# Optimization experiments

Measured on AMD Instinct MI355X. Metric: run time of the kernel, lower is better.

Reference implementation:

```python
import jax, jax.numpy as jnp
import numpy as np

N_NODES = 50000
N_EDGES = 800000
IN_CH, HID_CH, OUT_CH = 512, 256, 128


def setup_inputs() -> dict:
    key = jax.random.key(0)
    k = jax.random.split(key, 6)
    x = jax.random.normal(k[0], (N_NODES, IN_CH), dtype=jnp.float32)
    edge_index = jax.random.randint(k[1], (2, N_EDGES), 0, N_NODES, dtype=jnp.int64)
    # Glorot-ish scaled weights
    W0 = jax.random.normal(k[2], (IN_CH, HID_CH), dtype=jnp.float32) * (1.0 / np.sqrt(IN_CH))
    b0 = jnp.zeros((HID_CH,), dtype=jnp.float32)
    W1 = jax.random.normal(k[3], (HID_CH, OUT_CH), dtype=jnp.float32) * (1.0 / np.sqrt(HID_CH))
    b1 = jnp.zeros((OUT_CH,), dtype=jnp.float32)
    PW = jax.random.normal(k[4], (OUT_CH, OUT_CH), dtype=jnp.float32) * (1.0 / np.sqrt(OUT_CH))
    Pb = jnp.zeros((OUT_CH,), dtype=jnp.float32)
    return {"x": x, "edge_index": edge_index, "W0": W0, "b0": b0,
            "W1": W1, "b1": b1, "PW": PW, "Pb": Pb}


def reference(x, edge_index, W0, b0, W1, b1, PW, Pb):
    N = x.shape[0]
    # GCN normalization with added self-loops (edge_weight=None -> ones)
    loop = jnp.arange(N, dtype=edge_index.dtype)
    src = jnp.concatenate([edge_index[0], loop])  # [E+N]
    dst = jnp.concatenate([edge_index[1], loop])
    w = jnp.ones(src.shape[0], dtype=x.dtype)
    deg = jax.ops.segment_sum(w, dst, num_segments=N)  # in-degree incl. self-loop
    dinv = jnp.where(deg > 0, jax.lax.rsqrt(jnp.maximum(deg, 1e-12)), 0.0)
    norm = dinv[src] * dinv[dst]  # [E+N]

    def gcn_conv(h, W, b):
        hl = h @ W                               # [N, F_out] linear first (PyG GCNConv)
        msg = norm[:, None] * hl[src]            # gather + scale  [E+N, F_out]
        return jax.ops.segment_sum(msg, dst, num_segments=N) + b

    # eval mode: dropout is identity
    h = jax.nn.relu(gcn_conv(x, W0, b0))
    h = gcn_conv(h, W1, b1)                      # last layer: no relu
    p = h @ PW + Pb                              # PGE linear [N, OUT]
    vals = jnp.max(p, axis=0)                    # torch.max(dim=0) -> (values, indices)
    idx = jnp.argmax(p, axis=0)
    return (h, vals, idx)
```

## Files before the change

kernel.cpp:

```cpp
#include <hip/hip_runtime.h>
#include <stdint.h>

#define N_NODES 50000
#define N_EDGES 800000
#define IN_CH   512
#define HID_CH  256
#define OUT_CH  128
#define NPAD    50048
#define SLOT    96

#define NB_E   3125
#define NB2    391

#define PBKT  NB_E
#define PW0B  (PBKT + 64)
#define PW1B  (PW0B + 16)
#define PPWB  (PW1B + 8)

typedef unsigned short ushort_t;
typedef __attribute__((ext_vector_type(8))) short    short8;
typedef __attribute__((ext_vector_type(4))) float    floatx4;
typedef __attribute__((ext_vector_type(4))) _Float16 half4v;
typedef __attribute__((ext_vector_type(2))) _Float16 half2v;

__device__ inline ushort_t f2bf(float x) {
    union { float f; unsigned u; } v; v.f = x;
    unsigned r = v.u + 0x7fffu + ((v.u >> 16) & 1u);
    return (ushort_t)(r >> 16);
}
__device__ inline float bf2f(ushort_t h) {
    union { unsigned u; float f; } v; v.u = ((unsigned)h) << 16;
    return v.f;
}
__device__ inline void gl_lds16(const void* g, void* l) {
    __builtin_amdgcn_global_load_lds((const __attribute__((address_space(1))) void*)g,
                                     (__attribute__((address_space(3))) void*)l, 16, 0, 0);
}

#define SWZ(r) ((((r) >> 1) & 3) << 3)

#define SYNC_PIPE(N) do {                                                    \
    asm volatile("s_waitcnt vmcnt(" #N ") lgkmcnt(0)" ::: "memory");         \
    __builtin_amdgcn_sched_barrier(0);                                       \
    __builtin_amdgcn_s_barrier();                                            \
    __builtin_amdgcn_sched_barrier(0); } while (0)

__device__ inline void conv_splitT8(const float* __restrict__ W,
                                    ushort_t* __restrict__ WhT,
                                    ushort_t* __restrict__ WlT,
                                    int K, int N, int base) {
    float4 v0 = *(const float4*)(W + base);
    float4 v1 = *(const float4*)(W + base + 4);
    float vv[8] = {v0.x, v0.y, v0.z, v0.w, v1.x, v1.y, v1.z, v1.w};
    #pragma unroll
    for (int j = 0; j < 8; ++j) {
        int g = base + j;
        int k = g / N, n = g - k * N;
        int ks = k ^ SWZ(n);
        ushort_t h = f2bf(vv[j]);
        WhT[(size_t)n * K + ks] = h;
        WlT[(size_t)n * K + ks] = f2bf(vv[j] - bf2f(h));
    }
}

__global__ __launch_bounds__(256) void k_prep(const int* __restrict__ esrc,
                                              const int* __restrict__ edst,
                                              const float* __restrict__ W0,
                                              const float* __restrict__ W1,
                                              const float* __restrict__ PW,
                                              int* __restrict__ cnt,
                                              int* __restrict__ slots,
                                              ushort_t* W0hT, ushort_t* W0lT,
                                              ushort_t* W1hT, ushort_t* W1lT,
                                              ushort_t* PWhT, ushort_t* PWlT) {
    int b = blockIdx.x, tid = threadIdx.x;
    if (b < PBKT) {
        int e = b * 256 + tid;
        if (e < N_EDGES) {
            int d = edst[e];
            int c = atomicAdd(&cnt[d], 1);
            slots[(size_t)d * SLOT + c] = esrc[e];
        }
    } else if (b < PW0B) {
        conv_splitT8(W0, W0hT, W0lT, IN_CH, HID_CH, (b - PBKT) * 2048 + tid * 8);
    } else if (b < PW1B) {
        conv_splitT8(W1, W1hT, W1lT, HID_CH, OUT_CH, (b - PW0B) * 2048 + tid * 8);
    } else {
        conv_splitT8(PW, PWhT, PWlT, OUT_CH, OUT_CH, (b - PW1B) * 2048 + tid * 8);
    }
}

__global__ __launch_bounds__(256) void k_dinv(const int* __restrict__ cnt,
                                              float* __restrict__ dinv) {
    int i = blockIdx.x * 256 + threadIdx.x;
    if (i < N_NODES) dinv[i] = rsqrtf((float)cnt[i] + 1.0f);
}

__global__ __launch_bounds__(256, 2) void gemm0_x(const float* __restrict__ A,
                                                  const ushort_t* __restrict__ BhT,
                                                  const ushort_t* __restrict__ BlT,
                                                  const float* __restrict__ dinv,
                                                  _Float16* __restrict__ C,
                                                  int M, int N) {
    constexpr int KT = IN_CH;
    constexpr int NT = KT / 32;
    __shared__ ushort_t sm[2][4][128 * 32];
    const int tid  = threadIdx.x;
    const int wave = tid >> 6, lane = tid & 63;
    const int m0 = blockIdx.y * 128, n0 = blockIdx.x * 128;

    const int sr = tid >> 1, sseg = tid & 1;
    const float* gA = A + (size_t)min(m0 + sr, M - 1) * KT + sseg * 16;
    const int swa = (sr >> 1) & 3;
    const int wo0 = sr * 32 + (((sseg * 2)     ^ swa) * 8);
    const int wo1 = sr * 32 + (((sseg * 2 + 1) ^ swa) * 8);

    const int c0 = wave * 128 + lane, c1 = c0 + 64;
    const ushort_t* gbh0 = BhT + (size_t)(n0 + (c0 >> 2)) * KT + (c0 & 3) * 8;
    const ushort_t* gbh1 = BhT + (size_t)(n0 + (c1 >> 2)) * KT + (c1 & 3) * 8;
    const ushort_t* gbl0 = BlT + (size_t)(n0 + (c0 >> 2)) * KT + (c0 & 3) * 8;
    const ushort_t* gbl1 = BlT + (size_t)(n0 + (c1 >> 2)) * KT + (c1 & 3) * 8;
    const int lo0 = wave * 1024, lo1 = wave * 1024 + 512;

    float4 q0, q1, q2, q3;
    auto loadA = [&]() {
        q0 = ((const float4*)gA)[0]; q1 = ((const float4*)gA)[1];
        q2 = ((const float4*)gA)[2]; q3 = ((const float4*)gA)[3];
        gA += 32;
    };
    auto stageB = [&](int buf) {
        gl_lds16(gbh0, &sm[buf][2][lo0]); gl_lds16(gbh1, &sm[buf][2][lo1]);
        gl_lds16(gbl0, &sm[buf][3][lo0]); gl_lds16(gbl1, &sm[buf][3][lo1]);
        gbh0 += 32; gbh1 += 32; gbl0 += 32; gbl1 += 32;
    };
    auto splitpack = [](float a, float b, unsigned& hp, unsigned& lp) {
        unsigned ua = __float_as_uint(a), ub = __float_as_uint(b);
        unsigned hb = ub & 0xffff0000u;
        float ra = a - __uint_as_float(ua & 0xffff0000u);
        float rb = b - __uint_as_float(hb);
        hp = (ua >> 16) | hb;
        lp = (__float_as_uint(ra) >> 16) | (__float_as_uint(rb) & 0xffff0000u);
    };
    auto writeA = [&](int buf) {
        float vv[16] = {q0.x, q0.y, q0.z, q0.w, q1.x, q1.y, q1.z, q1.w,
                        q2.x, q2.y, q2.z, q2.w, q3.x, q3.y, q3.z, q3.w};
        unsigned hp[8], lp[8];
        #pragma unroll
        for (int j = 0; j < 8; ++j) splitpack(vv[2 * j], vv[2 * j + 1], hp[j], lp[j]);
        *(uint4*)&sm[buf][0][wo0] = make_uint4(hp[0], hp[1], hp[2], hp[3]);
        *(uint4*)&sm[buf][0][wo1] = make_uint4(hp[4], hp[5], hp[6], hp[7]);
        *(uint4*)&sm[buf][1][wo0] = make_uint4(lp[0], lp[1], lp[2], lp[3]);
        *(uint4*)&sm[buf][1][wo1] = make_uint4(lp[4], lp[5], lp[6], lp[7]);
    };

    floatx4 zero = {0.f, 0.f, 0.f, 0.f};
    floatx4 acc[4][4];
    #pragma unroll
    for (int i = 0; i < 4; ++i)
        #pragma unroll
        for (int j = 0; j < 4; ++j) acc[i][j] = zero;

    const int wm = (wave & 1) * 64, wn = (wave >> 1) * 64;
    const int fr = lane & 15, fq = lane >> 4;
    const int sx = SWZ(fr);

    loadA();
    stageB(0);
    writeA(0);
    loadA();
    asm volatile("s_waitcnt vmcnt(4) lgkmcnt(0)" ::: "memory");
    __builtin_amdgcn_sched_barrier(0);
    __builtin_amdgcn_s_barrier();
    __builtin_amdgcn_sched_barrier(0);

    #pragma unroll 2
    for (int t = 0; t < NT; ++t) {
        const int cur = t & 1, nxt = cur ^ 1;
        if (t + 1 < NT) stageB(nxt);
        short8 afh[4], afl[4], bfh[4], bfl[4];
        #pragma unroll
        for (int tt = 0; tt < 4; ++tt) {
            int ai = (wm + tt * 16 + fr) * 32 + (fq * 8 ^ sx);
            int bi = (wn + tt * 16 + fr) * 32 + (fq * 8 ^ sx);
            afh[tt] = *(const short8*)&sm[cur][0][ai];
            afl[tt] = *(const short8*)&sm[cur][1][ai];
            bfh[tt] = *(const short8*)&sm[cur][2][bi];
            bfl[tt] = *(const short8*)&sm[cur][3][bi];
        }
        if (t + 1 < NT) {
            writeA(nxt);
            __builtin_amdgcn_sched_barrier(0);
            if (t + 2 < NT) loadA();
        }
        #pragma unroll
        for (int i = 0; i < 4; ++i)
            #pragma unroll
            for (int j = 0; j < 4; ++j) {
                acc[i][j] = __builtin_amdgcn_mfma_f32_16x16x32_bf16(afh[i], bfh[j], acc[i][j], 0, 0, 0);
                acc[i][j] = __builtin_amdgcn_mfma_f32_16x16x32_bf16(afh[i], bfl[j], acc[i][j], 0, 0, 0);
                acc[i][j] = __builtin_amdgcn_mfma_f32_16x16x32_bf16(afl[i], bfh[j], acc[i][j], 0, 0, 0);
            }
        if (t + 1 < NT) {
            if (t + 2 < NT) SYNC_PIPE(4);
            else            SYNC_PIPE(0);
        }
    }
    const int colb = n0 + wn + fr;
    #pragma unroll
    for (int i = 0; i < 4; ++i) {
        int rowb = m0 + wm + i * 16 + fq * 4;
        #pragma unroll
        for (int r = 0; r < 4; ++r) {
            int row = rowb + r;
            if (row < M) {
                float dv = dinv[row];
                _Float16* cp = C + (size_t)row * N + colb;
                cp[0]  = (_Float16)(acc[i][0][r] * dv);
                cp[16] = (_Float16)(acc[i][1][r] * dv);
                cp[32] = (_Float16)(acc[i][2][r] * dv);
                cp[48] = (_Float16)(acc[i][3][r] * dv);
            }
        }
    }
}

template <int KT>
__global__ __launch_bounds__(256, 2) void gemm_bf(const ushort_t* __restrict__ Ah,
                                                  const ushort_t* __restrict__ Al,
                                                  const ushort_t* __restrict__ BhT,
                                                  const ushort_t* __restrict__ BlT,
                                                  const float* __restrict__ dinv,
                                                  _Float16* __restrict__ C,
                                                  int M, int N) {
    constexpr int NT = KT / 32;
    __shared__ ushort_t sm[2][4][128 * 32];
    const int tid  = threadIdx.x;
    const int wave = tid >> 6, lane = tid & 63;
    const int m0 = blockIdx.y * 128, n0 = blockIdx.x * 128;

    const int c0 = wave * 128 + lane, c1 = c0 + 64;
    const int ar0 = min(m0 + (c0 >> 2), M - 1), ar1 = min(m0 + (c1 >> 2), M - 1);
    const ushort_t* gah0 = Ah + (size_t)ar0 * KT + (c0 & 3) * 8;
    const ushort_t* gah1 = Ah + (size_t)ar1 * KT + (c1 & 3) * 8;
    const ushort_t* gal0 = Al + (size_t)ar0 * KT + (c0 & 3) * 8;
    const ushort_t* gal1 = Al + (size_t)ar1 * KT + (c1 & 3) * 8;
    const ushort_t* gbh0 = BhT + (size_t)(n0 + (c0 >> 2)) * KT + (c0 & 3) * 8;
    const ushort_t* gbh1 = BhT + (size_t)(n0 + (c1 >> 2)) * KT + (c1 & 3) * 8;
    const ushort_t* gbl0 = BlT + (size_t)(n0 + (c0 >> 2)) * KT + (c0 & 3) * 8;
    const ushort_t* gbl1 = BlT + (size_t)(n0 + (c1 >> 2)) * KT + (c1 & 3) * 8;
    const int lo0 = wave * 1024, lo1 = wave * 1024 + 512;

    auto stage = [&](int buf) {
        gl_lds16(gah0, &sm[buf][0][lo0]); gl_lds16(gah1, &sm[buf][0][lo1]);
        gl_lds16(gal0, &sm[buf][1][lo0]); gl_lds16(gal1, &sm[buf][1][lo1]);
        gl_lds16(gbh0, &sm[buf][2][lo0]); gl_lds16(gbh1, &sm[buf][2][lo1]);
        gl_lds16(gbl0, &sm[buf][3][lo0]); gl_lds16(gbl1, &sm[buf][3][lo1]);
        gah0 += 32; gah1 += 32; gal0 += 32; gal1 += 32;
        gbh0 += 32; gbh1 += 32; gbl0 += 32; gbl1 += 32;
    };

    floatx4 zero = {0.f, 0.f, 0.f, 0.f};
    floatx4 acc[4][4];
    #pragma unroll
    for (int i = 0; i < 4; ++i)
        #pragma unroll
        for (int j = 0; j < 4; ++j) acc[i][j] = zero;

    const int wm = (wave & 1) * 64, wn = (wave >> 1) * 64;
    const int fr = lane & 15, fq = lane >> 4;
    const int sx = SWZ(fr);

    stage(0);
    SYNC_PIPE(0);

    #pragma unroll 2
    for (int t = 0; t < NT; ++t) {
        const int cur = t & 1, nxt = cur ^ 1;
        if (t + 1 < NT) stage(nxt);
        short8 afh[4], afl[4], bfh[4], bfl[4];
        #pragma unroll
        for (int tt = 0; tt < 4; ++tt) {
            int ai = (wm + tt * 16 + fr) * 32 + (fq * 8 ^ sx);
            int bi = (wn + tt * 16 + fr) * 32 + (fq * 8 ^ sx);
            afh[tt] = *(const short8*)&sm[cur][0][ai];
            afl[tt] = *(const short8*)&sm[cur][1][ai];
            bfh[tt] = *(const short8*)&sm[cur][2][bi];
            bfl[tt] = *(const short8*)&sm[cur][3][bi];
        }
        #pragma unroll
        for (int i = 0; i < 4; ++i)
            #pragma unroll
            for (int j = 0; j < 4; ++j) {
                acc[i][j] = __builtin_amdgcn_mfma_f32_16x16x32_bf16(afh[i], bfh[j], acc[i][j], 0, 0, 0);
                acc[i][j] = __builtin_amdgcn_mfma_f32_16x16x32_bf16(afh[i], bfl[j], acc[i][j], 0, 0, 0);
                acc[i][j] = __builtin_amdgcn_mfma_f32_16x16x32_bf16(afl[i], bfh[j], acc[i][j], 0, 0, 0);
            }
        if (t + 1 < NT) SYNC_PIPE(0);
    }
    const int colb = n0 + wn + fr;
    #pragma unroll
    for (int i = 0; i < 4; ++i) {
        int rowb = m0 + wm + i * 16 + fq * 4;
        #pragma unroll
        for (int r = 0; r < 4; ++r) {
            int row = rowb + r;
            if (row < M) {
                float dv = dinv[row];
                _Float16* cp = C + (size_t)row * N + colb;
                cp[0]  = (_Float16)(acc[i][0][r] * dv);
                cp[16] = (_Float16)(acc[i][1][r] * dv);
                cp[32] = (_Float16)(acc[i][2][r] * dv);
                cp[48] = (_Float16)(acc[i][3][r] * dv);
            }
        }
    }
}

__global__ __launch_bounds__(256, 2) void gemm_pge(const ushort_t* __restrict__ Ah,
                                                   const ushort_t* __restrict__ Al,
                                                   const ushort_t* __restrict__ BhT,
                                                   const ushort_t* __restrict__ BlT,
                                                   float* __restrict__ pv,
                                                   int* __restrict__ pi,
                                                   int M) {
    constexpr int KT = OUT_CH;
    constexpr int NT = KT / 32;
    __shared__ ushort_t sm[2][4][128 * 32];
    __shared__ float redv[8][128];
    __shared__ int   redi[8][128];
    const int tid  = threadIdx.x;
    const int wave = tid >> 6, lane = tid & 63;
    const int m0 = blockIdx.x * 128;

    const int c0 = wave * 128 + lane, c1 = c0 + 64;
    const int ar0 = min(m0 + (c0 >> 2), M - 1), ar1 = min(m0 + (c1 >> 2), M - 1);
    const ushort_t* gah0 = Ah + (size_t)ar0 * KT + (c0 & 3) * 8;
    const ushort_t* gah1 = Ah + (size_t)ar1 * KT + (c1 & 3) * 8;
    const ushort_t* gal0 = Al + (size_t)ar0 * KT + (c0 & 3) * 8;
    const ushort_t* gal1 = Al + (size_t)ar1 * KT + (c1 & 3) * 8;
    const ushort_t* gbh0 = BhT + (size_t)(c0 >> 2) * KT + (c0 & 3) * 8;
    const ushort_t* gbh1 = BhT + (size_t)(c1 >> 2) * KT + (c1 & 3) * 8;
    const ushort_t* gbl0 = BlT + (size_t)(c0 >> 2) * KT + (c0 & 3) * 8;
    const ushort_t* gbl1 = BlT + (size_t)(c1 >> 2) * KT + (c1 & 3) * 8;
    const int lo0 = wave * 1024, lo1 = wave * 1024 + 512;

    auto stage = [&](int buf) {
        gl_lds16(gah0, &sm[buf][0][lo0]); gl_lds16(gah1, &sm[buf][0][lo1]);
        gl_lds16(gal0, &sm[buf][1][lo0]); gl_lds16(gal1, &sm[buf][1][lo1]);
        gl_lds16(gbh0, &sm[buf][2][lo0]); gl_lds16(gbh1, &sm[buf][2][lo1]);
        gl_lds16(gbl0, &sm[buf][3][lo0]); gl_lds16(gbl1, &sm[buf][3][lo1]);
        gah0 += 32; gah1 += 32; gal0 += 32; gal1 += 32;
        gbh0 += 32; gbh1 += 32; gbl0 += 32; gbl1 += 32;
    };

    floatx4 zero = {0.f, 0.f, 0.f, 0.f};
    floatx4 acc[4][4];
    #pragma unroll
    for (int i = 0; i < 4; ++i)
        #pragma unroll
        for (int j = 0; j < 4; ++j) acc[i][j] = zero;

    const int wm = (wave & 1) * 64, wn = (wave >> 1) * 64;
    const int fr = lane & 15, fq = lane >> 4;
    const int sx = SWZ(fr);

    stage(0);
    SYNC_PIPE(0);

    #pragma unroll 2
    for (int t = 0; t < NT; ++t) {
        const int cur = t & 1, nxt = cur ^ 1;
        if (t + 1 < NT) stage(nxt);
        short8 afh[4], afl[4], bfh[4], bfl[4];
        #pragma unroll
        for (int tt = 0; tt < 4; ++tt) {
            int ai = (wm + tt * 16 + fr) * 32 + (fq * 8 ^ sx);
            int bi = (wn + tt * 16 + fr) * 32 + (fq * 8 ^ sx);
            afh[tt] = *(const short8*)&sm[cur][0][ai];
            afl[tt] = *(const short8*)&sm[cur][1][ai];
            bfh[tt] = *(const short8*)&sm[cur][2][bi];
            bfl[tt] = *(const short8*)&sm[cur][3][bi];
        }
        #pragma unroll
        for (int i = 0; i < 4; ++i)
            #pragma unroll
            for (int j = 0; j < 4; ++j) {
                acc[i][j] = __builtin_amdgcn_mfma_f32_16x16x32_bf16(afh[i], bfh[j], acc[i][j], 0, 0, 0);
                acc[i][j] = __builtin_amdgcn_mfma_f32_16x16x32_bf16(afh[i], bfl[j], acc[i][j], 0, 0, 0);
                acc[i][j] = __builtin_amdgcn_mfma_f32_16x16x32_bf16(afl[i], bfh[j], acc[i][j], 0, 0, 0);
            }
        if (t + 1 < NT) SYNC_PIPE(0);
    }
    __syncthreads();
    const int slot = (wave & 1) * 4 + fq;
    #pragma unroll
    for (int j = 0; j < 4; ++j) {
        float bv = -3.402823466e+38f; int bidx = 0;
        #pragma unroll
        for (int i = 0; i < 4; ++i) {
            int rowb = m0 + wm + i * 16 + fq * 4;
            #pragma unroll
            for (int r = 0; r < 4; ++r) {
                int row = rowb + r;
                float v = acc[i][j][r];
                if (row < M && v > bv) { bv = v; bidx = row; }
            }
        }
        redv[slot][wn + j * 16 + fr] = bv;
        redi[slot][wn + j * 16 + fr] = bidx;
    }
    __syncthreads();
    if (tid < 128) {
        float bv = redv[0][tid]; int bidx = redi[0][tid];
        #pragma unroll
        for (int s = 1; s < 8; ++s) {
            float v = redv[s][tid]; int ix = redi[s][tid];
            if (v > bv || (v == bv && ix < bidx)) { bv = v; bidx = ix; }
        }
        pv[blockIdx.x * 128 + tid] = bv;
        pi[blockIdx.x * 128 + tid] = bidx;
    }
}

__global__ __launch_bounds__(128) void agg256_relu_bf(const _Float16* __restrict__ hl,
                                                      const float* __restrict__ dinv,
                                                      const int* __restrict__ cnt,
                                                      const int* __restrict__ slots,
                                                      const float* __restrict__ bias,
                                                      ushort_t* __restrict__ oh,
                                                      ushort_t* __restrict__ ol) {
    int d = blockIdx.x * 2 + (threadIdx.x >> 6);
    int lane = threadIdx.x & 63;
    float di = dinv[d];
    half4v v = ((const half4v*)(hl + (size_t)d * 256))[lane];
    float ax = (float)v[0], ay = (float)v[1], az = (float)v[2], aw = (float)v[3];
    const int* sl = slots + (size_t)d * SLOT;
    int n = cnt[d];
    for (int e = 0; e < n; e += 8) {
        int s[8]; float m[8]; half4v u[8];
        #pragma unroll
        for (int j = 0; j < 8; ++j) {
            bool live = (e + j) < n;
            s[j] = live ? sl[e + j] : d;
            m[j] = live ? 1.0f : 0.0f;
        }
        #pragma unroll
        for (int j = 0; j < 8; ++j) u[j] = ((const half4v*)(hl + (size_t)s[j] * 256))[lane];
        #pragma unroll
        for (int j = 0; j < 8; ++j) {
            ax += m[j] * (float)u[j][0]; ay += m[j] * (float)u[j][1];
            az += m[j] * (float)u[j][2]; aw += m[j] * (float)u[j][3];
        }
    }
    float4 b = ((const float4*)bias)[lane];
    float rx = fmaxf(fmaf(di, ax, b.x), 0.0f), ry = fmaxf(fmaf(di, ay, b.y), 0.0f);
    float rz = fmaxf(fmaf(di, az, b.z), 0.0f), rw = fmaxf(fmaf(di, aw, b.w), 0.0f);
    ushort4 hv, lv;
    hv.x = f2bf(rx); lv.x = f2bf(rx - bf2f(hv.x));
    hv.y = f2bf(ry); lv.y = f2bf(ry - bf2f(hv.y));
    hv.z = f2bf(rz); lv.z = f2bf(rz - bf2f(hv.z));
    hv.w = f2bf(rw); lv.w = f2bf(rw - bf2f(hv.w));
    int sidx = (lane * 4) ^ SWZ(d);
    *(ushort4*)&oh[(size_t)d * 256 + sidx] = hv;
    *(ushort4*)&ol[(size_t)d * 256 + sidx] = lv;
}

__global__ __launch_bounds__(128) void agg128_bias_bf(const _Float16* __restrict__ hl,
                                                      const float* __restrict__ dinv,
                                                      const int* __restrict__ cnt,
                                                      const int* __restrict__ slots,
                                                      const float* __restrict__ bias,
                                                      float* __restrict__ out,
                                                      ushort_t* __restrict__ oh,
                                                      ushort_t* __restrict__ ol) {
    int d = blockIdx.x * 2 + (threadIdx.x >> 6);
    int lane = threadIdx.x & 63;
    float di = dinv[d];
    half2v v = ((const half2v*)(hl + (size_t)d * 128))[lane];
    float ax = (float)v[0], ay = (float)v[1];
    const int* sl = slots + (size_t)d * SLOT;
    int n = cnt[d];
    for (int e = 0; e < n; e += 8) {
        int s[8]; float m[8]; half2v u[8];
        #pragma unroll
        for (int j = 0; j < 8; ++j) {
            bool live = (e + j) < n;
            s[j] = live ? sl[e + j] : d;
            m[j] = live ? 1.0f : 0.0f;
        }
        #pragma unroll
        for (int j = 0; j < 8; ++j) u[j] = ((const half2v*)(hl + (size_t)s[j] * 128))[lane];
        #pragma unroll
        for (int j = 0; j < 8; ++j) { ax += m[j] * (float)u[j][0]; ay += m[j] * (float)u[j][1]; }
    }
    float2 b = ((const float2*)bias)[lane];
    float rx = fmaf(di, ax, b.x), ry = fmaf(di, ay, b.y);
    ((float2*)(out + (size_t)d * 128))[lane] = make_float2(rx, ry);
    ushort2 hv, lv;
    hv.x = f2bf(rx); lv.x = f2bf(rx - bf2f(hv.x));
    hv.y = f2bf(ry); lv.y = f2bf(ry - bf2f(hv.y));
    int sidx = (lane * 2) ^ SWZ(d);
    *(ushort2*)&oh[(size_t)d * 128 + sidx] = hv;
    *(ushort2*)&ol[(size_t)d * 128 + sidx] = lv;
}

__global__ __launch_bounds__(256) void k_reduce2(const float* __restrict__ pv,
                                                 const int* __restrict__ pi,
                                                 const float* __restrict__ Pb,
                                                 float* __restrict__ out) {
    int c = threadIdx.x & 127, sub = threadIdx.x >> 7;
    float best = -3.402823466e+38f;
    int bi = 0;
    for (int b = sub; b < NB2; b += 2) {
        float v = pv[b * 128 + c];
        int ix = pi[b * 128 + c];
        if (v > best || (v == best && ix < bi)) { best = v; bi = ix; }
    }
    __shared__ float sv[128];
    __shared__ int   si[128];
    if (sub == 1) { sv[c] = best; si[c] = bi; }
    __syncthreads();
    if (sub == 0) {
        float v1 = sv[c]; int i1 = si[c];
        if (v1 > best || (v1 == best && i1 < bi)) { best = v1; bi = i1; }
        out[(size_t)N_NODES * OUT_CH + c]       = best + Pb[c];
        out[(size_t)N_NODES * OUT_CH + 128 + c] = (float)bi;
    }
}

extern "C" void kernel_launch(void* const* d_in, const int* in_sizes, int n_in,
                              void* d_out, int out_size, void* d_ws, size_t ws_size,
                              hipStream_t stream) {
    const float* x  = (const float*)d_in[0];
    const int*   ei = (const int*)d_in[1];
    const float* W0 = (const float*)d_in[2];
    const float* b0 = (const float*)d_in[3];
    const float* W1 = (const float*)d_in[4];
    const float* b1 = (const float*)d_in[5];
    const float* PW = (const float*)d_in[6];
    const float* Pb = (const float*)d_in[7];
    float* out = (float*)d_out;
    const int* esrc = ei;
    const int* edst = ei + N_EDGES;

    char* w = (char*)d_ws;
    size_t off = 0;
    auto alloc = [&](size_t bytes) -> void* {
        void* p = (void*)(w + off);
        off = (off + bytes + 255) & ~(size_t)255;
        return p;
    };
    int*       cnt    = (int*)alloc((size_t)N_NODES * 4);
    float*     dinv   = (float*)alloc((size_t)N_NODES * 4);
    int*       slots  = (int*)alloc((size_t)N_NODES * SLOT * 4);
    float*     pmax_v = (float*)alloc((size_t)NB2 * 128 * 4);
    int*       pmax_i = (int*)alloc((size_t)NB2 * 128 * 4);
    _Float16*  bufH   = (_Float16*)alloc((size_t)NPAD * 256 * 2);
    ushort_t*  h0h    = (ushort_t*)alloc((size_t)N_NODES * HID_CH * 2);
    ushort_t*  h0l    = (ushort_t*)alloc((size_t)N_NODES * HID_CH * 2);
    ushort_t*  h1h    = (ushort_t*)alloc((size_t)N_NODES * OUT_CH * 2);
    ushort_t*  h1l    = (ushort_t*)alloc((size_t)N_NODES * OUT_CH * 2);
    ushort_t*  W0hT   = (ushort_t*)alloc((size_t)IN_CH * HID_CH * 2);
    ushort_t*  W0lT   = (ushort_t*)alloc((size_t)IN_CH * HID_CH * 2);
    ushort_t*  W1hT   = (ushort_t*)alloc((size_t)HID_CH * OUT_CH * 2);
    ushort_t*  W1lT   = (ushort_t*)alloc((size_t)HID_CH * OUT_CH * 2);
    ushort_t*  PWhT   = (ushort_t*)alloc((size_t)OUT_CH * OUT_CH * 2);
    ushort_t*  PWlT   = (ushort_t*)alloc((size_t)OUT_CH * OUT_CH * 2);

    hipMemsetAsync(cnt, 0, (size_t)N_NODES * 4, stream);
    k_prep<<<PPWB, 256, 0, stream>>>(esrc, edst, W0, W1, PW, cnt, slots,
                                     W0hT, W0lT, W1hT, W1lT, PWhT, PWlT);
    k_dinv<<<196, 256, 0, stream>>>(cnt, dinv);

    gemm0_x<<<dim3(HID_CH / 128, NB2), 256, 0, stream>>>(
        x, W0hT, W0lT, dinv, bufH, N_NODES, HID_CH);
    agg256_relu_bf<<<N_NODES / 2, 128, 0, stream>>>(bufH, dinv, cnt, slots, b0, h0h, h0l);

    gemm_bf<HID_CH><<<dim3(1, NB2), 256, 0, stream>>>(
        h0h, h0l, W1hT, W1lT, dinv, bufH, N_NODES, OUT_CH);
    agg128_bias_bf<<<N_NODES / 2, 128, 0, stream>>>(bufH, dinv, cnt, slots, b1,
                                                    out, h1h, h1l);

    gemm_pge<<<NB2, 256, 0, stream>>>(h1h, h1l, PWhT, PWlT, pmax_v, pmax_i, N_NODES);
    k_reduce2<<<1, 256, 0, stream>>>(pmax_v, pmax_i, Pb, out);

    (void)in_sizes; (void)n_in; (void)out_size; (void)ws_size;
}
```

Baseline: 461.5 us.

## Drop double-buffering in GEMMs and stage fp32 A tile directly to LDS

Replaces the double-buffered LDS pipelines in all three GEMM kernels with single-buffer load, barrier, compute, barrier loops. This halves shared memory use and raises the occupancy hint for gemm0_x to 3 blocks. In gemm0_x the fp32 A tile is now copied straight into padded LDS with global_load_lds, and the bf16 hi/lo split happens when fragments are read rather than during a register-staged write. The cost is that global load latency is no longer hidden behind MFMA work within a block, so the kernels depend on higher occupancy to cover it. gemm0_x also repeats the split work per wave, and the fp32 A tile takes more LDS read bandwidth than the packed bf16 tiles did.

```diff
diff --git a/kernel.cpp b/kernel.cpp
--- a/kernel.cpp
+++ b/kernel.cpp
@@ -11,6 +11,7 @@
 
 #define NB_E   3125
 #define NB2    391
+#define AP     36
 
 #define PBKT  NB_E
 #define PW0B  (PBKT + 64)
@@ -38,12 +39,6 @@
 }
 
 #define SWZ(r) ((((r) >> 1) & 3) << 3)
-
-#define SYNC_PIPE(N) do {                                                    \
-    asm volatile("s_waitcnt vmcnt(" #N ") lgkmcnt(0)" ::: "memory");         \
-    __builtin_amdgcn_sched_barrier(0);                                       \
-    __builtin_amdgcn_s_barrier();                                            \
-    __builtin_amdgcn_sched_barrier(0); } while (0)
 
 __device__ inline void conv_splitT8(const float* __restrict__ W,
                                     ushort_t* __restrict__ WhT,
@@ -96,7 +91,7 @@
     if (i < N_NODES) dinv[i] = rsqrtf((float)cnt[i] + 1.0f);
 }
 
-__global__ __launch_bounds__(256, 2) void gemm0_x(const float* __restrict__ A,
+__global__ __launch_bounds__(256, 3) void gemm0_x(const float* __restrict__ A,
                                                   const ushort_t* __restrict__ BhT,
                                                   const ushort_t* __restrict__ BlT,
                                                   const float* __restrict__ dinv,
@@ -104,54 +99,33 @@
                                                   int M, int N) {
     constexpr int KT = IN_CH;
     constexpr int NT = KT / 32;
-    __shared__ ushort_t sm[2][4][128 * 32];
+    __shared__ float    smA[128 * AP];
+    __shared__ ushort_t smB[2][128 * 32];
     const int tid  = threadIdx.x;
     const int wave = tid >> 6, lane = tid & 63;
     const int m0 = blockIdx.y * 128, n0 = blockIdx.x * 128;
 
-    const int sr = tid >> 1, sseg = tid & 1;
-    const float* gA = A + (size_t)min(m0 + sr, M - 1) * KT + sseg * 16;
-    const int swa = (sr >> 1) & 3;
-    const int wo0 = sr * 32 + (((sseg * 2)     ^ swa) * 8);
-    const int wo1 = sr * 32 + (((sseg * 2 + 1) ^ swa) * 8);
+    const float* psrc[5];
+    float*       adst[5];
+    #pragma unroll
+    for (int i = 0; i < 5; ++i) {
+        int c = wave + 4 * i;
+        int cc = (c < 18) ? c : 0;
+        int p = cc * 256 + lane * 4;
+        int r = p / AP, col = p - r * AP;
+        int gr = min(m0 + r, M - 1);
+        int gc = (col < 32) ? col : 0;
+        psrc[i] = A + (size_t)gr * KT + gc;
+        adst[i] = smA + cc * 256;
+    }
 
     const int c0 = wave * 128 + lane, c1 = c0 + 64;
     const ushort_t* gbh0 = BhT + (size_t)(n0 + (c0 >> 2)) * KT + (c0 & 3) * 8;
     const ushort_t* gbh1 = BhT + (size_t)(n0 + (c1 >> 2)) * KT + (c1 & 3) * 8;
     const ushort_t* gbl0 = BlT + (size_t)(n0 + (c0 >> 2)) * KT + (c0 & 3) * 8;
     const ushort_t* gbl1 = BlT + (size_t)(n0 + (c1 >> 2)) * KT + (c1 & 3) * 8;
-    const int lo0 = wave * 1024, lo1 = wave * 1024 + 512;
-
-    float4 q0, q1, q2, q3;
-    auto loadA = [&]() {
-        q0 = ((const float4*)gA)[0]; q1 = ((const float4*)gA)[1];
-        q2 = ((const float4*)gA)[2]; q3 = ((const float4*)gA)[3];
-        gA += 32;
-    };
-    auto stageB = [&](int buf) {
-        gl_lds16(gbh0, &sm[buf][2][lo0]); gl_lds16(gbh1, &sm[buf][2][lo1]);
-        gl_lds16(gbl0, &sm[buf][3][lo0]); gl_lds16(gbl1, &sm[buf][3][lo1]);
-        gbh0 += 32; gbh1 += 32; gbl0 += 32; gbl1 += 32;
-    };
-    auto splitpack = [](float a, float b, unsigned& hp, unsigned& lp) {
-        unsigned ua = __float_as_uint(a), ub = __float_as_uint(b);
-        unsigned hb = ub & 0xffff0000u;
-        float ra = a - __uint_as_float(ua & 0xffff0000u);
-        float rb = b - __uint_as_float(hb);
-        hp = (ua >> 16) | hb;
-        lp = (__float_as_uint(ra) >> 16) | (__float_as_uint(rb) & 0xffff0000u);
-    };
-    auto writeA = [&](int buf) {
-        float vv[16] = {q0.x, q0.y, q0.z, q0.w, q1.x, q1.y, q1.z, q1.w,
-                        q2.x, q2.y, q2.z, q2.w, q3.x, q3.y, q3.z, q3.w};
-        unsigned hp[8], lp[8];
-        #pragma unroll
-        for (int j = 0; j < 8; ++j) splitpack(vv[2 * j], vv[2 * j + 1], hp[j], lp[j]);
-        *(uint4*)&sm[buf][0][wo0] = make_uint4(hp[0], hp[1], hp[2], hp[3]);
-        *(uint4*)&sm[buf][0][wo1] = make_uint4(hp[4], hp[5], hp[6], hp[7]);
-        *(uint4*)&sm[buf][1][wo0] = make_uint4(lp[0], lp[1], lp[2], lp[3]);
-        *(uint4*)&sm[buf][1][wo1] = make_uint4(lp[4], lp[5], lp[6], lp[7]);
-    };
+    ushort_t* lb0 = &smB[0][wave * 1024];  ushort_t* lb1 = &smB[0][wave * 1024 + 512];
+    ushort_t* lc0 = &smB[1][wave * 1024];  ushort_t* lc1 = &smB[1][wave * 1024 + 512];
 
     floatx4 zero = {0.f, 0.f, 0.f, 0.f};
     floatx4 acc[4][4];
@@ -164,33 +138,36 @@
     const int fr = lane & 15, fq = lane >> 4;
     const int sx = SWZ(fr);
 
-    loadA();
-    stageB(0);
-    writeA(0);
-    loadA();
-    asm volatile("s_waitcnt vmcnt(4) lgkmcnt(0)" ::: "memory");
-    __builtin_amdgcn_sched_barrier(0);
-    __builtin_amdgcn_s_barrier();
-    __builtin_amdgcn_sched_barrier(0);
-
-    #pragma unroll 2
     for (int t = 0; t < NT; ++t) {
-        const int cur = t & 1, nxt = cur ^ 1;
-        if (t + 1 < NT) stageB(nxt);
+        #pragma unroll
+        for (int i = 0; i < 5; ++i)
+            if (wave + 4 * i < 18) { gl_lds16(psrc[i], adst[i]); psrc[i] += 32; }
+        gl_lds16(gbh0, lb0); gl_lds16(gbh1, lb1);
+        gl_lds16(gbl0, lc0); gl_lds16(gbl1, lc1);
+        gbh0 += 32; gbh1 += 32; gbl0 += 32; gbl1 += 32;
+        __syncthreads();
         short8 afh[4], afl[4], bfh[4], bfl[4];
         #pragma unroll
         for (int tt = 0; tt < 4; ++tt) {
-            int ai = (wm + tt * 16 + fr) * 32 + (fq * 8 ^ sx);
+            const float* ap = &smA[(wm + tt * 16 + fr) * AP + fq * 8];
+            float4 v0 = *(const float4*)ap;
+            float4 v1 = *(const float4*)(ap + 4);
+            float f[8] = {v0.x, v0.y, v0.z, v0.w, v1.x, v1.y, v1.z, v1.w};
+            union { unsigned u[4]; short8 v; } hh, ll;
+            #pragma unroll
+            for (int j = 0; j < 4; ++j) {
+                unsigned ua = __float_as_uint(f[2 * j]);
+                unsigned ub = __float_as_uint(f[2 * j + 1]);
+                unsigned ha = ua & 0xffff0000u, hb = ub & 0xffff0000u;
+                hh.u[j] = (ha >> 16) | hb;
+                float ra = f[2 * j]     - __uint_as_float(ha);
+                float rb = f[2 * j + 1] - __uint_as_float(hb);
+                ll.u[j] = (__float_as_uint(ra) >> 16) | (__float_as_uint(rb) & 0xffff0000u);
+            }
+            afh[tt] = hh.v; afl[tt] = ll.v;
             int bi = (wn + tt * 16 + fr) * 32 + (fq * 8 ^ sx);
-            afh[tt] = *(const short8*)&sm[cur][0][ai];
-            afl[tt] = *(const short8*)&sm[cur][1][ai];
-            bfh[tt] = *(const short8*)&sm[cur][2][bi];
-            bfl[tt] = *(const short8*)&sm[cur][3][bi];
-        }
-        if (t + 1 < NT) {
-            writeA(nxt);
-            __builtin_amdgcn_sched_barrier(0);
-            if (t + 2 < NT) loadA();
+            bfh[tt] = *(const short8*)&smB[0][bi];
+            bfl[tt] = *(const short8*)&smB[1][bi];
         }
         #pragma unroll
         for (int i = 0; i < 4; ++i)
@@ -200,10 +177,7 @@
                 acc[i][j] = __builtin_amdgcn_mfma_f32_16x16x32_bf16(afh[i], bfl[j], acc[i][j], 0, 0, 0);
                 acc[i][j] = __builtin_amdgcn_mfma_f32_16x16x32_bf16(afl[i], bfh[j], acc[i][j], 0, 0, 0);
             }
-        if (t + 1 < NT) {
-            if (t + 2 < NT) SYNC_PIPE(4);
-            else            SYNC_PIPE(0);
-        }
+        __syncthreads();
     }
     const int colb = n0 + wn + fr;
     #pragma unroll
@@ -225,15 +199,15 @@
 }
 
 template <int KT>
-__global__ __launch_bounds__(256, 2) void gemm_bf(const ushort_t* __restrict__ Ah,
-                                                  const ushort_t* __restrict__ Al,
-                                                  const ushort_t* __restrict__ BhT,
-                                                  const ushort_t* __restrict__ BlT,
-                                                  const float* __restrict__ dinv,
-                                                  _Float16* __restrict__ C,
-                                                  int M, int N) {
+__global__ __launch_bounds__(256) void gemm_bf(const ushort_t* __restrict__ Ah,
+                                               const ushort_t* __restrict__ Al,
+                                               const ushort_t* __restrict__ BhT,
+                                               const ushort_t* __restrict__ BlT,
+                                               const float* __restrict__ dinv,
+                                               _Float16* __restrict__ C,
+                                               int M, int N) {
     constexpr int NT = KT / 32;
-    __shared__ ushort_t sm[2][4][128 * 32];
+    __shared__ ushort_t sm[4][128 * 32];
     const int tid  = threadIdx.x;
     const int wave = tid >> 6, lane = tid & 63;
     const int m0 = blockIdx.y * 128, n0 = blockIdx.x * 128;
@@ -248,16 +222,10 @@
     const ushort_t* gbh1 = BhT + (size_t)(n0 + (c1 >> 2)) * KT + (c1 & 3) * 8;
     const ushort_t* gbl0 = BlT + (size_t)(n0 + (c0 >> 2)) * KT + (c0 & 3) * 8;
     const ushort_t* gbl1 = BlT + (size_t)(n0 + (c1 >> 2)) * KT + (c1 & 3) * 8;
-    const int lo0 = wave * 1024, lo1 = wave * 1024 + 512;
-
-    auto stage = [&](int buf) {
-        gl_lds16(gah0, &sm[buf][0][lo0]); gl_lds16(gah1, &sm[buf][0][lo1]);
-        gl_lds16(gal0, &sm[buf][1][lo0]); gl_lds16(gal1, &sm[buf][1][lo1]);
-        gl_lds16(gbh0, &sm[buf][2][lo0]); gl_lds16(gbh1, &sm[buf][2][lo1]);
-        gl_lds16(gbl0, &sm[buf][3][lo0]); gl_lds16(gbl1, &sm[buf][3][lo1]);
-        gah0 += 32; gah1 += 32; gal0 += 32; gal1 += 32;
-        gbh0 += 32; gbh1 += 32; gbl0 += 32; gbl1 += 32;
-    };
+    ushort_t* la0 = &sm[0][wave * 1024];       ushort_t* la1 = &sm[0][wave * 1024 + 512];
+    ushort_t* ll0 = &sm[1][wave * 1024];       ushort_t* ll1 = &sm[1][wave * 1024 + 512];
+    ushort_t* lb0 = &sm[2][wave * 1024];       ushort_t* lb1 = &sm[2][wave * 1024 + 512];
+    ushort_t* lc0 = &sm[3][wave * 1024];       ushort_t* lc1 = &sm[3][wave * 1024 + 512];
 
     floatx4 zero = {0.f, 0.f, 0.f, 0.f};
     floatx4 acc[4][4];
@@ -270,22 +238,23 @@
     const int fr = lane & 15, fq = lane >> 4;
     const int sx = SWZ(fr);
 
-    stage(0);
-    SYNC_PIPE(0);
-
-    #pragma unroll 2
     for (int t = 0; t < NT; ++t) {
-        const int cur = t & 1, nxt = cur ^ 1;
-        if (t + 1 < NT) stage(nxt);
+        gl_lds16(gah0, la0); gl_lds16(gah1, la1);
+        gl_lds16(gal0, ll0); gl_lds16(gal1, ll1);
+        gl_lds16(gbh0, lb0); gl_lds16(gbh1, lb1);
+        gl_lds16(gbl0, lc0); gl_lds16(gbl1, lc1);
+        gah0 += 32; gah1 += 32; gal0 += 32; gal1 += 32;
+        gbh0 += 32; gbh1 += 32; gbl0 += 32; gbl1 += 32;
+        __syncthreads();
         short8 afh[4], afl[4], bfh[4], bfl[4];
         #pragma unroll
         for (int tt = 0; tt < 4; ++tt) {
             int ai = (wm + tt * 16 + fr) * 32 + (fq * 8 ^ sx);
             int bi = (wn + tt * 16 + fr) * 32 + (fq * 8 ^ sx);
-            afh[tt] = *(const short8*)&sm[cur][0][ai];
-            afl[tt] = *(const short8*)&sm[cur][1][ai];
-            bfh[tt] = *(const short8*)&sm[cur][2][bi];
-            bfl[tt] = *(const short8*)&sm[cur][3][bi];
+            afh[tt] = *(const short8*)&sm[0][ai];
+            afl[tt] = *(const short8*)&sm[1][ai];
+            bfh[tt] = *(const short8*)&sm[2][bi];
+            bfl[tt] = *(const short8*)&sm[3][bi];
         }
         #pragma unroll
         for (int i = 0; i < 4; ++i)
@@ -295,7 +264,7 @@
                 acc[i][j] = __builtin_amdgcn_mfma_f32_16x16x32_bf16(afh[i], bfl[j], acc[i][j], 0, 0, 0);
                 acc[i][j] = __builtin_amdgcn_mfma_f32_16x16x32_bf16(afl[i], bfh[j], acc[i][j], 0, 0, 0);
             }
-        if (t + 1 < NT) SYNC_PIPE(0);
+        __syncthreads();
     }
     const int colb = n0 + wn + fr;
     #pragma unroll
@@ -316,16 +285,16 @@
     }
 }
 
-__global__ __launch_bounds__(256, 2) void gemm_pge(const ushort_t* __restrict__ Ah,
-                                                   const ushort_t* __restrict__ Al,
-                                                   const ushort_t* __restrict__ BhT,
-                                                   const ushort_t* __restrict__ BlT,
-                                                   float* __restrict__ pv,
-                                                   int* __restrict__ pi,
-                                                   int M) {
+__global__ __launch_bounds__(256) void gemm_pge(const ushort_t* __restrict__ Ah,
+                                                const ushort_t* __restrict__ Al,
+                                                const ushort_t* __restrict__ BhT,
+                                                const ushort_t* __restrict__ BlT,
+                                                float* __restrict__ pv,
+                                                int* __restrict__ pi,
+                                                int M) {
     constexpr int KT = OUT_CH;
     constexpr int NT = KT / 32;
-    __shared__ ushort_t sm[2][4][128 * 32];
+    __shared__ ushort_t sm[4][128 * 32];
     __shared__ float redv[8][128];
     __shared__ int   redi[8][128];
     const int tid  = threadIdx.x;
@@ -342,16 +311,10 @@
     const ushort_t* gbh1 = BhT + (size_t)(c1 >> 2) * KT + (c1 & 3) * 8;
     const ushort_t* gbl0 = BlT + (size_t)(c0 >> 2) * KT + (c0 & 3) * 8;
     const ushort_t* gbl1 = BlT + (size_t)(c1 >> 2) * KT + (c1 & 3) * 8;
-    const int lo0 = wave * 1024, lo1 = wave * 1024 + 512;
-
-    auto stage = [&](int buf) {
-        gl_lds16(gah0, &sm[buf][0][lo0]); gl_lds16(gah1, &sm[buf][0][lo1]);
-        gl_lds16(gal0, &sm[buf][1][lo0]); gl_lds16(gal1, &sm[buf][1][lo1]);
-        gl_lds16(gbh0, &sm[buf][2][lo0]); gl_lds16(gbh1, &sm[buf][2][lo1]);
-        gl_lds16(gbl0, &sm[buf][3][lo0]); gl_lds16(gbl1, &sm[buf][3][lo1]);
-        gah0 += 32; gah1 += 32; gal0 += 32; gal1 += 32;
-        gbh0 += 32; gbh1 += 32; gbl0 += 32; gbl1 += 32;
-    };
+    ushort_t* la0 = &sm[0][wave * 1024];       ushort_t* la1 = &sm[0][wave * 1024 + 512];
+    ushort_t* ll0 = &sm[1][wave * 1024];       ushort_t* ll1 = &sm[1][wave * 1024 + 512];
+    ushort_t* lb0 = &sm[2][wave * 1024];       ushort_t* lb1 = &sm[2][wave * 1024 + 512];
+    ushort_t* lc0 = &sm[3][wave * 1024];       ushort_t* lc1 = &sm[3][wave * 1024 + 512];
 
     floatx4 zero = {0.f, 0.f, 0.f, 0.f};
     floatx4 acc[4][4];
@@ -364,22 +327,23 @@
     const int fr = lane & 15, fq = lane >> 4;
     const int sx = SWZ(fr);
 
-    stage(0);
-    SYNC_PIPE(0);
-
-    #pragma unroll 2
     for (int t = 0; t < NT; ++t) {
-        const int cur = t & 1, nxt = cur ^ 1;
-        if (t + 1 < NT) stage(nxt);
+        gl_lds16(gah0, la0); gl_lds16(gah1, la1);
+        gl_lds16(gal0, ll0); gl_lds16(gal1, ll1);
+        gl_lds16(gbh0, lb0); gl_lds16(gbh1, lb1);
+        gl_lds16(gbl0, lc0); gl_lds16(gbl1, lc1);
+        gah0 += 32; gah1 += 32; gal0 += 32; gal1 += 32;
+        gbh0 += 32; gbh1 += 32; gbl0 += 32; gbl1 += 32;
+        __syncthreads();
         short8 afh[4], afl[4], bfh[4], bfl[4];
         #pragma unroll
         for (int tt = 0; tt < 4; ++tt) {
             int ai = (wm + tt * 16 + fr) * 32 + (fq * 8 ^ sx);
             int bi = (wn + tt * 16 + fr) * 32 + (fq * 8 ^ sx);
-            afh[tt] = *(const short8*)&sm[cur][0][ai];
-            afl[tt] = *(const short8*)&sm[cur][1][ai];
-            bfh[tt] = *(const short8*)&sm[cur][2][bi];
-            bfl[tt] = *(const short8*)&sm[cur][3][bi];
+            afh[tt] = *(const short8*)&sm[0][ai];
+            afl[tt] = *(const short8*)&sm[1][ai];
+            bfh[tt] = *(const short8*)&sm[2][bi];
+            bfl[tt] = *(const short8*)&sm[3][bi];
         }
         #pragma unroll
         for (int i = 0; i < 4; ++i)
@@ -389,9 +353,8 @@
                 acc[i][j] = __builtin_amdgcn_mfma_f32_16x16x32_bf16(afh[i], bfl[j], acc[i][j], 0, 0, 0);
                 acc[i][j] = __builtin_amdgcn_mfma_f32_16x16x32_bf16(afl[i], bfh[j], acc[i][j], 0, 0, 0);
             }
-        if (t + 1 < NT) SYNC_PIPE(0);
-    }
-    __syncthreads();
+        __syncthreads();
+    }
     const int slot = (wave & 1) * 4 + fq;
     #pragma unroll
     for (int j = 0; j < 4; ++j) {
```

Result: no change. 452.8 us (-1.9%).
